# Performance work log

Measured on AMD Instinct MI355X. Metric: run time of the kernel, lower is better.

Reference implementation:

```python
import jax, jax.numpy as jnp
import numpy as np


def setup_inputs() -> dict:
    key = jax.random.key(0)
    kq, kk, kv = jax.random.split(key, 3)
    B, H, S, D = 4, 16, 2048, 64
    query = jax.random.normal(kq, (B, H, S, D), dtype=jnp.float32)
    key_t = jax.random.normal(kk, (B, H, S, D), dtype=jnp.float32)
    value = jax.random.normal(kv, (B, H, S, D), dtype=jnp.float32)
    return {"query": query, "key": key_t, "value": value}


def reference(query, key, value):
    # score = Q K^T / sqrt(dk)   -> [B, H, S, S]
    dk = jnp.asarray(query.shape[-1], dtype=query.dtype)
    score = jnp.einsum("bhqd,bhkd->bhqk", query, key) / jnp.sqrt(dk)
    # relu activation instead of softmax (no mask: source mask branch is
    # unreachable/buggy; dropout rate 0.0 -> identity)
    attn_weights = jax.nn.relu(score)
    context = jnp.einsum("bhqk,bhkd->bhqd", attn_weights, value)
    return (context, attn_weights)
```

## Files before the change

### kernel.cpp

```cpp
#include <hip/hip_runtime.h>


typedef __attribute__((ext_vector_type(4))) float f32x4;
typedef __attribute__((ext_vector_type(8))) short bf16x8;
typedef __attribute__((ext_vector_type(4))) short bf16x4;

#define S_LEN 2048
#define D_HEAD 64
#define KST 72

__device__ __forceinline__ short f2bf(float x) {
  union { float f; unsigned u; } v; v.f = x;
  unsigned r = v.u + 0x7fffu + ((v.u >> 16) & 1u);
  return (short)(r >> 16);
}

__device__ __forceinline__ bf16x8 cvt8(f32x4 a, f32x4 b) {
  bf16x8 r;
  r[0] = f2bf(a[0]); r[1] = f2bf(a[1]); r[2] = f2bf(a[2]); r[3] = f2bf(a[3]);
  r[4] = f2bf(b[0]); r[5] = f2bf(b[1]); r[6] = f2bf(b[2]); r[7] = f2bf(b[3]);
  return r;
}

__global__ void ScaledDotProductAttention_40166534152796_kernel(
    const float* __restrict__ Q, const float* __restrict__ K,
    const float* __restrict__ V, float* __restrict__ ctx,
    float* __restrict__ attn) {
  __shared__ short Kb[64 * KST];
  __shared__ short Vt[64 * KST];
  __shared__ short Pb[128 * KST];

  const int tid = threadIdx.x;
  const int wave = tid >> 6;
  const int lane = tid & 63;
  const int t = lane & 15;
  const int quad = lane >> 4;

  const int qblk = blockIdx.x;
  const int bh = blockIdx.y;

  const float* Qh = Q + (size_t)bh * S_LEN * D_HEAD;
  const float* Kh = K + (size_t)bh * S_LEN * D_HEAD;
  const float* Vh = V + (size_t)bh * S_LEN * D_HEAD;
  float* ctxh = ctx + (size_t)bh * S_LEN * D_HEAD;
  float* attnh = attn + (size_t)bh * S_LEN * S_LEN;

  bf16x8 qfrag[2][2];
#pragma unroll
  for (int qc = 0; qc < 2; ++qc) {
#pragma unroll
    for (int s = 0; s < 2; ++s) {
      const int qrow = qblk * 128 + wave * 32 + qc * 16 + t;
      const f32x4* p = (const f32x4*)(Qh + qrow * D_HEAD + s * 32 + quad * 8);
      f32x4 a = p[0], b = p[1];
      a *= 0.125f; b *= 0.125f;
      qfrag[qc][s] = cvt8(a, b);
    }
  }

  const int srow = tid >> 2;
  const int dseg = (tid & 3) * 16;

  f32x4 acc_c[2][4];
#pragma unroll
  for (int r = 0; r < 2; ++r)
#pragma unroll
    for (int c = 0; c < 4; ++c) acc_c[r][c] = (f32x4)(0.0f);

  for (int kt = 0; kt < 32; ++kt) {
    __syncthreads();

    {
      const f32x4* kp = (const f32x4*)(Kh + (size_t)(kt * 64 + srow) * D_HEAD + dseg);
      f32x4 k0 = kp[0], k1 = kp[1], k2 = kp[2], k3 = kp[3];
      *(bf16x8*)&Kb[srow * KST + dseg] = cvt8(k0, k1);
      *(bf16x8*)&Kb[srow * KST + dseg + 8] = cvt8(k2, k3);

      const f32x4* vp = (const f32x4*)(Vh + (size_t)(kt * 64 + srow) * D_HEAD + dseg);
      f32x4 v0 = vp[0], v1 = vp[1], v2 = vp[2], v3 = vp[3];
      float vv[16];
#pragma unroll
      for (int j = 0; j < 4; ++j) { vv[j] = v0[j]; vv[4 + j] = v1[j]; vv[8 + j] = v2[j]; vv[12 + j] = v3[j]; }
#pragma unroll
      for (int j = 0; j < 16; ++j) Vt[(dseg + j) * KST + srow] = f2bf(vv[j]);
    }
    __syncthreads();

    bf16x8 afr[4][2];
#pragma unroll
    for (int kr = 0; kr < 4; ++kr)
#pragma unroll
      for (int s = 0; s < 2; ++s)
        afr[kr][s] = *(const bf16x8*)&Kb[(kr * 16 + t) * KST + s * 32 + quad * 8];

    f32x4 sa[4][2];
#pragma unroll
    for (int kr = 0; kr < 4; ++kr)
#pragma unroll
      for (int qc = 0; qc < 2; ++qc) sa[kr][qc] = (f32x4)(0.0f);

#pragma unroll
    for (int s = 0; s < 2; ++s)
#pragma unroll
      for (int kr = 0; kr < 4; ++kr)
#pragma unroll
        for (int qc = 0; qc < 2; ++qc)
          sa[kr][qc] = __builtin_amdgcn_mfma_f32_16x16x32_bf16(
              afr[kr][s], qfrag[qc][s], sa[kr][qc], 0, 0, 0);

#pragma unroll
    for (int kr = 0; kr < 4; ++kr) {
#pragma unroll
      for (int qc = 0; qc < 2; ++qc) {
        f32x4 v = sa[kr][qc];
#pragma unroll
        for (int i = 0; i < 4; ++i) v[i] = fmaxf(v[i], 0.0f);
        const int qg = qblk * 128 + wave * 32 + qc * 16 + t;
        const int key = kt * 64 + kr * 16 + quad * 4;
        *(f32x4*)(attnh + (size_t)qg * S_LEN + key) = v;
        bf16x4 pv;
#pragma unroll
        for (int i = 0; i < 4; ++i) pv[i] = f2bf(v[i]);
        *(bf16x4*)&Pb[(wave * 32 + qc * 16 + t) * KST + kr * 16 + quad * 4] = pv;
      }
    }

#pragma unroll
    for (int s2 = 0; s2 < 2; ++s2) {
      bf16x8 pa[2], vb[4];
#pragma unroll
      for (int r = 0; r < 2; ++r)
        pa[r] = *(const bf16x8*)&Pb[(wave * 32 + r * 16 + t) * KST + s2 * 32 + quad * 8];
#pragma unroll
      for (int c = 0; c < 4; ++c)
        vb[c] = *(const bf16x8*)&Vt[(c * 16 + t) * KST + s2 * 32 + quad * 8];
#pragma unroll
      for (int r = 0; r < 2; ++r)
#pragma unroll
        for (int c = 0; c < 4; ++c)
          acc_c[r][c] = __builtin_amdgcn_mfma_f32_16x16x32_bf16(
              pa[r], vb[c], acc_c[r][c], 0, 0, 0);
    }
  }

#pragma unroll
  for (int r = 0; r < 2; ++r) {
#pragma unroll
    for (int c = 0; c < 4; ++c) {
#pragma unroll
      for (int i = 0; i < 4; ++i) {
        const int qg = qblk * 128 + wave * 32 + r * 16 + quad * 4 + i;
        const int d = c * 16 + t;
        ctxh[(size_t)qg * D_HEAD + d] = acc_c[r][c][i];
      }
    }
  }
}

extern "C" void kernel_launch(void* const* d_in, const int* in_sizes, int n_in,
                              void* d_out, int out_size, void* d_ws, size_t ws_size,
                              hipStream_t stream) {
  const float* Q = (const float*)d_in[0];
  const float* K = (const float*)d_in[1];
  const float* V = (const float*)d_in[2];
  float* ctx = (float*)d_out;
  float* attn = (float*)d_out + (size_t)4 * 16 * 2048 * 64;

  dim3 grid(16, 64, 1);
  dim3 block(256, 1, 1);
  ScaledDotProductAttention_40166534152796_kernel<<<grid, block, 0, stream>>>(
      Q, K, V, ctx, attn);
}
```

Baseline: 1.386 ms.

## Pre-convert Q/K/V to bf16 and double-buffer K/V tiles via direct LDS loads

New measurement: 1.363 ms. About the same (-1.7%).

```diff
diff --git a/kernel.cpp b/kernel.cpp
--- a/kernel.cpp
+++ b/kernel.cpp
@@ -3,95 +3,146 @@
 
 typedef __attribute__((ext_vector_type(4))) float f32x4;
 typedef __attribute__((ext_vector_type(8))) short bf16x8;
-typedef __attribute__((ext_vector_type(4))) short bf16x4;
+typedef __attribute__((ext_vector_type(2))) unsigned u32x2;
 
 #define S_LEN 2048
 #define D_HEAD 64
-#define KST 72
-
-__device__ __forceinline__ short f2bf(float x) {
-  union { float f; unsigned u; } v; v.f = x;
-  unsigned r = v.u + 0x7fffu + ((v.u >> 16) & 1u);
-  return (short)(r >> 16);
-}
-
-__device__ __forceinline__ bf16x8 cvt8(f32x4 a, f32x4 b) {
-  bf16x8 r;
-  r[0] = f2bf(a[0]); r[1] = f2bf(a[1]); r[2] = f2bf(a[2]); r[3] = f2bf(a[3]);
-  r[4] = f2bf(b[0]); r[5] = f2bf(b[1]); r[6] = f2bf(b[2]); r[7] = f2bf(b[3]);
+#define NELEM 8388608
+
+__device__ __forceinline__ unsigned pkbf(float a, float b) {
+  unsigned r;
+  asm("v_cvt_pk_bf16_f32 %0, %1, %2" : "=v"(r) : "v"(a), "v"(b));
   return r;
 }
 
-__global__ void ScaledDotProductAttention_40166534152796_kernel(
+__device__ __forceinline__ bf16x8 pack8(f32x4 a, f32x4 b) {
+  union { unsigned u[4]; bf16x8 v; } r;
+  r.u[0] = pkbf(a[0], a[1]); r.u[1] = pkbf(a[2], a[3]);
+  r.u[2] = pkbf(b[0], b[1]); r.u[3] = pkbf(b[2], b[3]);
+  return r.v;
+}
+
+__device__ __forceinline__ void gload16(const void* g, void* l) {
+  __builtin_amdgcn_global_load_lds(
+      (const __attribute__((address_space(1))) unsigned int*)g,
+      (__attribute__((address_space(3))) unsigned int*)l, 16, 0, 0);
+}
+
+__global__ __launch_bounds__(256) void sdpa_prep_kernel(
     const float* __restrict__ Q, const float* __restrict__ K,
-    const float* __restrict__ V, float* __restrict__ ctx,
+    const float* __restrict__ V, short* __restrict__ Qb,
+    short* __restrict__ Kb, short* __restrict__ Vt) {
+  const int tid = threadIdx.x;
+  if (blockIdx.x < 2048) {
+    const size_t N8 = NELEM / 8;
+    for (size_t i = (size_t)blockIdx.x * 256 + tid; i < 2 * N8; i += (size_t)2048 * 256) {
+      const float* src; short* dst; float sc; size_t j;
+      if (i < N8) { src = Q; dst = Qb; sc = 0.125f; j = i; }
+      else        { src = K; dst = Kb; sc = 1.0f;   j = i - N8; }
+      const f32x4* p = (const f32x4*)(src + j * 8);
+      f32x4 a = p[0] * sc, b = p[1] * sc;
+      *(bf16x8*)(dst + j * 8) = pack8(a, b);
+    }
+  } else {
+    __shared__ short tile[64 * 72];
+    const int bid = blockIdx.x - 2048;
+    const int st = bid & 31, bh = bid >> 5;
+    const float* Vh = V + ((size_t)bh * S_LEN + st * 64) * D_HEAD;
+    const int r = tid >> 2, c0 = (tid & 3) * 16;
+    const f32x4* p = (const f32x4*)(Vh + r * D_HEAD + c0);
+    f32x4 a = p[0], b = p[1], c = p[2], d = p[3];
+    *(bf16x8*)&tile[r * 72 + c0] = pack8(a, b);
+    *(bf16x8*)&tile[r * 72 + c0 + 8] = pack8(c, d);
+    __syncthreads();
+    union { short s[8]; bf16x8 v; } o0, o1;
+#pragma unroll
+    for (int j = 0; j < 8; ++j) o0.s[j] = tile[(c0 + j) * 72 + r];
+#pragma unroll
+    for (int j = 0; j < 8; ++j) o1.s[j] = tile[(c0 + 8 + j) * 72 + r];
+    short* out = Vt + ((size_t)bh * D_HEAD + r) * S_LEN + st * 64 + c0;
+    *(bf16x8*)out = o0.v;
+    *(bf16x8*)(out + 8) = o1.v;
+  }
+}
+
+__global__ __launch_bounds__(256, 3) void ScaledDotProductAttention_40166534152796_kernel(
+    const short* __restrict__ Qb, const short* __restrict__ Kb,
+    const short* __restrict__ Vt, float* __restrict__ ctx,
     float* __restrict__ attn) {
-  __shared__ short Kb[64 * KST];
-  __shared__ short Vt[64 * KST];
-  __shared__ short Pb[128 * KST];
+  __shared__ __align__(128) char lds[49152];
+  char* ldsK = lds;
+  char* ldsV = lds + 16384;
+  char* ldsP = lds + 32768;
 
   const int tid = threadIdx.x;
   const int wave = tid >> 6;
   const int lane = tid & 63;
   const int t = lane & 15;
   const int quad = lane >> 4;
+  const int sw = (t & 7) << 4;
 
   const int qblk = blockIdx.x;
   const int bh = blockIdx.y;
 
-  const float* Qh = Q + (size_t)bh * S_LEN * D_HEAD;
-  const float* Kh = K + (size_t)bh * S_LEN * D_HEAD;
-  const float* Vh = V + (size_t)bh * S_LEN * D_HEAD;
-  float* ctxh = ctx + (size_t)bh * S_LEN * D_HEAD;
-  float* attnh = attn + (size_t)bh * S_LEN * S_LEN;
+  const short* Qh = Qb + (size_t)bh * (S_LEN * D_HEAD);
+  const char* Kh = (const char*)(Kb + (size_t)bh * (S_LEN * D_HEAD));
+  const char* Vh = (const char*)(Vt + (size_t)bh * (S_LEN * D_HEAD));
+  float* ctxh = ctx + (size_t)bh * (S_LEN * D_HEAD);
+  float* attnh = attn + (size_t)bh * ((size_t)S_LEN * S_LEN);
 
   bf16x8 qfrag[2][2];
 #pragma unroll
-  for (int qc = 0; qc < 2; ++qc) {
+  for (int qc = 0; qc < 2; ++qc)
 #pragma unroll
     for (int s = 0; s < 2; ++s) {
       const int qrow = qblk * 128 + wave * 32 + qc * 16 + t;
-      const f32x4* p = (const f32x4*)(Qh + qrow * D_HEAD + s * 32 + quad * 8);
-      f32x4 a = p[0], b = p[1];
-      a *= 0.125f; b *= 0.125f;
-      qfrag[qc][s] = cvt8(a, b);
-    }
-  }
-
-  const int srow = tid >> 2;
-  const int dseg = (tid & 3) * 16;
-
-  f32x4 acc_c[2][4];
-#pragma unroll
-  for (int r = 0; r < 2; ++r)
-#pragma unroll
-    for (int c = 0; c < 4; ++c) acc_c[r][c] = (f32x4)(0.0f);
+      qfrag[qc][s] = *(const bf16x8*)(Qh + qrow * D_HEAD + s * 32 + quad * 8);
+    }
+
+  int koff[2], voff[2];
+#pragma unroll
+  for (int i = 0; i < 2; ++i) {
+    const int o = wave * 2048 + i * 1024 + lane * 16;
+    const int r = o >> 7;
+    const int bs = (o & 127) ^ ((r & 7) << 4);
+    koff[i] = r * 128 + bs;
+    voff[i] = r * 4096 + bs;
+  }
+
+  f32x4 accT[4][2];
+#pragma unroll
+  for (int c = 0; c < 4; ++c)
+#pragma unroll
+    for (int r = 0; r < 2; ++r) accT[c][r] = (f32x4)(0.0f);
+
+#pragma unroll
+  for (int i = 0; i < 2; ++i) {
+    gload16(Kh + koff[i], ldsK + wave * 2048 + i * 1024);
+    gload16(Vh + voff[i], ldsV + wave * 2048 + i * 1024);
+  }
 
   for (int kt = 0; kt < 32; ++kt) {
+    const int bsel = (kt & 1) * 8192;
     __syncthreads();
 
-    {
-      const f32x4* kp = (const f32x4*)(Kh + (size_t)(kt * 64 + srow) * D_HEAD + dseg);
-      f32x4 k0 = kp[0], k1 = kp[1], k2 = kp[2], k3 = kp[3];
-      *(bf16x8*)&Kb[srow * KST + dseg] = cvt8(k0, k1);
-      *(bf16x8*)&Kb[srow * KST + dseg + 8] = cvt8(k2, k3);
-
-      const f32x4* vp = (const f32x4*)(Vh + (size_t)(kt * 64 + srow) * D_HEAD + dseg);
-      f32x4 v0 = vp[0], v1 = vp[1], v2 = vp[2], v3 = vp[3];
-      float vv[16];
-#pragma unroll
-      for (int j = 0; j < 4; ++j) { vv[j] = v0[j]; vv[4 + j] = v1[j]; vv[8 + j] = v2[j]; vv[12 + j] = v3[j]; }
-#pragma unroll
-      for (int j = 0; j < 16; ++j) Vt[(dseg + j) * KST + srow] = f2bf(vv[j]);
-    }
-    __syncthreads();
-
+    if (kt < 31) {
+      const int nsel = ((kt + 1) & 1) * 8192;
+      const size_t kg = (size_t)(kt + 1) * 8192;
+      const size_t vg = (size_t)(kt + 1) * 128;
+#pragma unroll
+      for (int i = 0; i < 2; ++i) {
+        gload16(Kh + kg + koff[i], ldsK + nsel + wave * 2048 + i * 1024);
+        gload16(Vh + vg + voff[i], ldsV + nsel + wave * 2048 + i * 1024);
+      }
+    }
+
+    const char* Kt_ = ldsK + bsel;
     bf16x8 afr[4][2];
 #pragma unroll
     for (int kr = 0; kr < 4; ++kr)
 #pragma unroll
       for (int s = 0; s < 2; ++s)
-        afr[kr][s] = *(const bf16x8*)&Kb[(kr * 16 + t) * KST + s * 32 + quad * 8];
+        afr[kr][s] = *(const bf16x8*)(Kt_ + (kr * 16 + t) * 128 + ((s * 64 + quad * 16) ^ sw));
 
     f32x4 sa[4][2];
 #pragma unroll
@@ -99,6 +150,7 @@
 #pragma unroll
       for (int qc = 0; qc < 2; ++qc) sa[kr][qc] = (f32x4)(0.0f);
 
+    __builtin_amdgcn_s_setprio(1);
 #pragma unroll
     for (int s = 0; s < 2; ++s)
 #pragma unroll
@@ -107,54 +159,53 @@
         for (int qc = 0; qc < 2; ++qc)
           sa[kr][qc] = __builtin_amdgcn_mfma_f32_16x16x32_bf16(
               afr[kr][s], qfrag[qc][s], sa[kr][qc], 0, 0, 0);
-
-#pragma unroll
-    for (int kr = 0; kr < 4; ++kr) {
+    __builtin_amdgcn_s_setprio(0);
+
+#pragma unroll
+    for (int kr = 0; kr < 4; ++kr)
 #pragma unroll
       for (int qc = 0; qc < 2; ++qc) {
         f32x4 v = sa[kr][qc];
 #pragma unroll
         for (int i = 0; i < 4; ++i) v[i] = fmaxf(v[i], 0.0f);
         const int qg = qblk * 128 + wave * 32 + qc * 16 + t;
-        const int key = kt * 64 + kr * 16 + quad * 4;
-        *(f32x4*)(attnh + (size_t)qg * S_LEN + key) = v;
-        bf16x4 pv;
-#pragma unroll
-        for (int i = 0; i < 4; ++i) pv[i] = f2bf(v[i]);
-        *(bf16x4*)&Pb[(wave * 32 + qc * 16 + t) * KST + kr * 16 + quad * 4] = pv;
+        __builtin_nontemporal_store(
+            v, (f32x4*)(attnh + (size_t)qg * S_LEN + kt * 64 + kr * 16 + quad * 4));
+        u32x2 pw;
+        pw[0] = pkbf(v[0], v[1]);
+        pw[1] = pkbf(v[2], v[3]);
+        *(u32x2*)(ldsP + (wave * 32 + qc * 16 + t) * 128 + ((kr * 32 + quad * 8) ^ sw)) = pw;
       }
-    }
-
+
+    const char* Vt_ = ldsV + bsel;
+    __builtin_amdgcn_s_setprio(1);
 #pragma unroll
     for (int s2 = 0; s2 < 2; ++s2) {
-      bf16x8 pa[2], vb[4];
+      bf16x8 vb[4], pa[2];
+#pragma unroll
+      for (int c = 0; c < 4; ++c)
+        vb[c] = *(const bf16x8*)(Vt_ + (c * 16 + t) * 128 + ((s2 * 64 + quad * 16) ^ sw));
 #pragma unroll
       for (int r = 0; r < 2; ++r)
-        pa[r] = *(const bf16x8*)&Pb[(wave * 32 + r * 16 + t) * KST + s2 * 32 + quad * 8];
+        pa[r] = *(const bf16x8*)(ldsP + (wave * 32 + r * 16 + t) * 128 +
+                                 ((s2 * 64 + quad * 16) ^ sw));
 #pragma unroll
       for (int c = 0; c < 4; ++c)
-        vb[c] = *(const bf16x8*)&Vt[(c * 16 + t) * KST + s2 * 32 + quad * 8];
-#pragma unroll
-      for (int r = 0; r < 2; ++r)
-#pragma unroll
-        for (int c = 0; c < 4; ++c)
-          acc_c[r][c] = __builtin_amdgcn_mfma_f32_16x16x32_bf16(
-              pa[r], vb[c], acc_c[r][c], 0, 0, 0);
-    }
-  }
-
-#pragma unroll
-  for (int r = 0; r < 2; ++r) {
+#pragma unroll
+        for (int r = 0; r < 2; ++r)
+          accT[c][r] = __builtin_amdgcn_mfma_f32_16x16x32_bf16(
+              vb[c], pa[r], accT[c][r], 0, 0, 0);
+    }
+    __builtin_amdgcn_s_setprio(0);
+  }
+
+#pragma unroll
+  for (int r = 0; r < 2; ++r)
 #pragma unroll
     for (int c = 0; c < 4; ++c) {
-#pragma unroll
-      for (int i = 0; i < 4; ++i) {
-        const int qg = qblk * 128 + wave * 32 + r * 16 + quad * 4 + i;
-        const int d = c * 16 + t;
-        ctxh[(size_t)qg * D_HEAD + d] = acc_c[r][c][i];
-      }
-    }
-  }
+      const int qg = qblk * 128 + wave * 32 + r * 16 + t;
+      *(f32x4*)(ctxh + (size_t)qg * D_HEAD + c * 16 + quad * 4) = accT[c][r];
+    }
 }
 
 extern "C" void kernel_launch(void* const* d_in, const int* in_sizes, int n_in,
@@ -164,10 +215,13 @@
   const float* K = (const float*)d_in[1];
   const float* V = (const float*)d_in[2];
   float* ctx = (float*)d_out;
-  float* attn = (float*)d_out + (size_t)4 * 16 * 2048 * 64;
-
-  dim3 grid(16, 64, 1);
-  dim3 block(256, 1, 1);
-  ScaledDotProductAttention_40166534152796_kernel<<<grid, block, 0, stream>>>(
-      Q, K, V, ctx, attn);
-}
+  float* attn = (float*)d_out + (size_t)NELEM;
+
+  short* Qb = (short*)d_ws;
+  short* Kb = Qb + (size_t)NELEM;
+  short* Vt = Kb + (size_t)NELEM;
+
+  sdpa_prep_kernel<<<dim3(4096, 1, 1), dim3(256, 1, 1), 0, stream>>>(Q, K, V, Qb, Kb, Vt);
+  ScaledDotProductAttention_40166534152796_kernel<<<dim3(16, 64, 1), dim3(256, 1, 1), 0,
+                                                    stream>>>(Qb, Kb, Vt, ctx, attn);
+}
```
